# Performance work log

Measured on AMD Instinct MI355X. Metric: run time of the kernel, lower is better.

The kernel has to match this reference:

```python
import jax, jax.numpy as jnp
import numpy as np

NUM_ITERS = 5
TEMP = 0.1


def setup_inputs() -> dict:
    key = jax.random.key(0)
    k1, k2 = jax.random.split(key)
    pred_masks = jax.random.uniform(k1, (1, 100, 512, 512), dtype=jnp.float32)
    gt_masks = jax.random.uniform(k2, (50, 512, 512), dtype=jnp.float32)
    return {"pred_masks": pred_masks, "gt_masks": gt_masks}


def reference(pred_masks, gt_masks):
    # pred_masks: [B=1, K, H, W]; gt_masks: [N, H, W]
    gt = gt_masks[None]  # [1, N, H, W]
    # cost[b,k,n] = 1 - <pred_k, gt_n> over HW
    cost = 1.0 - jnp.einsum('bkhw,bnhw->bkn', pred_masks, gt)
    log_alpha = -cost / TEMP  # [1, K, N]
    for _ in range(NUM_ITERS):
        log_alpha = log_alpha - jax.nn.logsumexp(log_alpha, axis=2, keepdims=True)
        log_alpha = log_alpha - jax.nn.logsumexp(log_alpha, axis=1, keepdims=True)
    return jnp.exp(log_alpha)
```

## Files before the change

### kernel.cpp

```cpp
#include <hip/hip_runtime.h>
#include <math.h>

#define HW       262144
#define TOTSTEPS (HW / 32)
#define MROWS    100
#define NCOLS    50
#define OUTSZ    (MROWS * NCOLS)

typedef __attribute__((ext_vector_type(8))) _Float16 f16x8;
typedef __attribute__((ext_vector_type(2))) __fp16   fp16x2;
typedef __attribute__((ext_vector_type(4))) float    f32x4;

#define ABYTES   14336
#define BUFBYTES 22528

typedef __attribute__((address_space(1))) const unsigned int GU32;
typedef __attribute__((address_space(3))) unsigned int LU32;

__device__ __forceinline__ void split_f16(const float4& v0, const float4& v1,
                                          f16x8& hi, f16x8& lo) {
  float xs[8] = {v0.x, v0.y, v0.z, v0.w, v1.x, v1.y, v1.z, v1.w};
  union { fp16x2 p[4]; f16x8 v; } H, L;
#pragma unroll
  for (int j = 0; j < 4; ++j) {
    H.p[j] = __builtin_amdgcn_cvt_pkrtz(xs[2 * j], xs[2 * j + 1]);
    float l0 = xs[2 * j]     - (float)H.p[j][0];
    float l1 = xs[2 * j + 1] - (float)H.p[j][1];
    L.p[j] = __builtin_amdgcn_cvt_pkrtz(l0, l1);
  }
  hi = H.v; lo = L.v;
}

__global__ __launch_bounds__(256, 3) void dm_phase1(
    const float* __restrict__ pred, const float* __restrict__ gt,
    float* __restrict__ partial, int nblk) {
  __shared__ unsigned char smem[2 * BUFBYTES];

  const int b    = blockIdx.x;
  const int tid  = threadIdx.x;
  const int lane = tid & 63;
  const int wid  = tid >> 6;
  const int wi = wid >> 1, wj = wid & 1;
  const int g = lane >> 4, r = lane & 15;

  const int k0s = (int)(((long)b * TOTSTEPS) / nblk);
  const int k1s = (int)(((long)(b + 1) * TOTSTEPS) / nblk);
  const int nst = k1s - k0s;

  const float* srcb[6];
#pragma unroll
  for (int it = 0; it < 6; ++it) {
    int s = (it < 5) ? it * 256 + tid : 1280 + tid;
    const float* p;
    if (s < 896) {
      int row = s >> 3, t = s & 7;
      int rr = row < MROWS ? row : MROWS - 1;
      p = pred + (size_t)rr * HW + ((t ^ (row & 7)) << 2);
    } else {
      int s2 = s - 896;
      int row = s2 >> 3, t = s2 & 7;
      int rr = row < NCOLS ? row : NCOLS - 1;
      p = gt + (size_t)rr * HW + ((t ^ (row & 7)) << 2);
    }
    srcb[it] = p;
  }

  auto STAGE = [&](int q, int kf) {
    unsigned char* bufb = smem + q * BUFBYTES;
#pragma unroll
    for (int it = 0; it < 5; ++it)
      __builtin_amdgcn_global_load_lds((GU32*)(srcb[it] + kf),
          (LU32*)(bufb + (it * 256 + wid * 64) * 16), 16, 0, 0);
    if (wid < 2)
      __builtin_amdgcn_global_load_lds((GU32*)(srcb[5] + kf),
          (LU32*)(bufb + (1280 + wid * 64) * 16), 16, 0, 0);
  };

  f32x4 acc[4][2] = {};

  auto COMPUTE = [&](int q) {
    const unsigned char* bufb = smem + q * BUFBYTES;
    f16x8 bh[2], bl[2];
#pragma unroll
    for (int nf = 0; nf < 2; ++nf) {
      int R = wj * 32 + nf * 16 + r;
      const unsigned char* rowb = bufb + ABYTES + R * 128;
      float4 v0 = *(const float4*)(rowb + (((2 * g    ) ^ (r & 7)) << 4));
      float4 v1 = *(const float4*)(rowb + (((2 * g + 1) ^ (r & 7)) << 4));
      split_f16(v0, v1, bh[nf], bl[nf]);
    }
#pragma unroll
    for (int mf = 0; mf < 4; ++mf) {
      if (wi == 0 || mf < 3) {
        int R = wi * 64 + mf * 16 + r;
        const unsigned char* rowb = bufb + R * 128;
        float4 v0 = *(const float4*)(rowb + (((2 * g    ) ^ (r & 7)) << 4));
        float4 v1 = *(const float4*)(rowb + (((2 * g + 1) ^ (r & 7)) << 4));
        f16x8 ah, al;
        split_f16(v0, v1, ah, al);
#pragma unroll
        for (int nf = 0; nf < 2; ++nf) {
          acc[mf][nf] = __builtin_amdgcn_mfma_f32_16x16x32_f16(ah, bh[nf], acc[mf][nf], 0, 0, 0);
          acc[mf][nf] = __builtin_amdgcn_mfma_f32_16x16x32_f16(al, bh[nf], acc[mf][nf], 0, 0, 0);
          acc[mf][nf] = __builtin_amdgcn_mfma_f32_16x16x32_f16(ah, bl[nf], acc[mf][nf], 0, 0, 0);
        }
      }
    }
  };

  STAGE(0, k0s << 5);
  asm volatile("s_waitcnt vmcnt(0)" ::: "memory");
  __builtin_amdgcn_s_barrier();

  int q = 0;
  for (int s = 0; s < nst; ++s) {
    if (s + 1 < nst) STAGE(q ^ 1, (k0s + s + 1) << 5);
    COMPUTE(q);
    if (s + 1 < nst) asm volatile("s_waitcnt vmcnt(0)" ::: "memory");
    __builtin_amdgcn_s_barrier();
    q ^= 1;
  }

#pragma unroll
  for (int mf = 0; mf < 4; ++mf) {
#pragma unroll
    for (int nf = 0; nf < 2; ++nf) {
#pragma unroll
      for (int qq = 0; qq < 4; ++qq) {
        int row = wi * 64 + mf * 16 + g * 4 + qq;
        int col = wj * 32 + nf * 16 + r;
        if (row < MROWS && col < NCOLS)
          partial[(size_t)b * OUTSZ + row * NCOLS + col] = acc[mf][nf][qq];
      }
    }
  }
}

template <int NB>
__global__ void dm_reduce(const float* __restrict__ partial,
                          double* __restrict__ la0) {
  const int tid = threadIdx.x, wid = tid >> 6, lane = tid & 63;
  const int pbase = blockIdx.x * 16 + wid * 4;
  if (pbase >= OUTSZ) return;
  constexpr int IT = NB / 64;
  float4 v[IT];
#pragma unroll
  for (int i = 0; i < IT; ++i)
    v[i] = *(const float4*)(partial + (size_t)(lane + 64 * i) * OUTSZ + pbase);
  double d0 = 0, d1 = 0, d2 = 0, d3 = 0;
#pragma unroll
  for (int i = 0; i < IT; ++i) {
    d0 += (double)v[i].x; d1 += (double)v[i].y;
    d2 += (double)v[i].z; d3 += (double)v[i].w;
  }
#pragma unroll
  for (int off = 32; off; off >>= 1) {
    d0 += __shfl_xor(d0, off);
    d1 += __shfl_xor(d1, off);
    d2 += __shfl_xor(d2, off);
    d3 += __shfl_xor(d3, off);
  }
  if (lane == 0) {
    la0[pbase + 0] = (d0 - 1.0) * 10.0;
    la0[pbase + 1] = (d1 - 1.0) * 10.0;
    la0[pbase + 2] = (d2 - 1.0) * 10.0;
    la0[pbase + 3] = (d3 - 1.0) * 10.0;
  }
}

__global__ __launch_bounds__(256) void dm_sinkhorn(const double* __restrict__ la_in,
                                                   float* __restrict__ out) {
  __shared__ double la[OUTSZ];
  __shared__ double rp[MROWS];
  __shared__ double cp[NCOLS];
  const int t = threadIdx.x;
  for (int p = t; p < OUTSZ; p += 256) la[p] = la_in[p];
  if (t < NCOLS) cp[t] = 0.0;
  __syncthreads();
  for (int it = 0; it < 5; ++it) {
    if (t < 2 * MROWS) {
      int row = t >> 1, sl = t & 1;
      double m = -1e300;
      for (int j = sl; j < NCOLS; j += 2) m = fmax(m, la[row * NCOLS + j] - cp[j]);
      float s = 0.f;
      for (int j = sl; j < NCOLS; j += 2)
        s += __expf((float)(la[row * NCOLS + j] - cp[j] - m));
      double mo = __shfl_xor(m, 1); float so = __shfl_xor(s, 1);
      double mn = fmax(m, mo);
      s = s * __expf((float)(m - mn)) + so * __expf((float)(mo - mn));
      if (sl == 0) rp[row] = mn + (double)__logf(s);
    }
    __syncthreads();
    if (t < 4 * NCOLS) {
      int col = t >> 2, sl = t & 3;
      double m = -1e300;
      for (int i = sl; i < MROWS; i += 4) m = fmax(m, la[i * NCOLS + col] - rp[i]);
      float s = 0.f;
      for (int i = sl; i < MROWS; i += 4)
        s += __expf((float)(la[i * NCOLS + col] - rp[i] - m));
#pragma unroll
      for (int off = 1; off < 4; off <<= 1) {
        double mo = __shfl_xor(m, off); float so = __shfl_xor(s, off);
        double mn = fmax(m, mo);
        s = s * __expf((float)(m - mn)) + so * __expf((float)(mo - mn));
        m = mn;
      }
      if (sl == 0) cp[col] = m + (double)__logf(s);
    }
    __syncthreads();
  }
  for (int p = t; p < OUTSZ; p += 256)
    out[p] = __expf((float)(la[p] - rp[p / NCOLS] - cp[p % NCOLS]));
}

extern "C" void kernel_launch(void* const* d_in, const int* in_sizes, int n_in,
                              void* d_out, int out_size, void* d_ws, size_t ws_size,
                              hipStream_t stream) {
  const float* pred = (const float*)d_in[0];
  const float* gt   = (const float*)d_in[1];
  float* out = (float*)d_out;

  auto fits = [&](int nb) {
    return ((size_t)nb * OUTSZ * sizeof(float) + OUTSZ * sizeof(double)) <= ws_size;
  };
  int nblk = fits(768) ? 768 : (fits(512) ? 512 : 256);

  float*  partial = (float*)d_ws;
  double* la0 = (double*)((char*)d_ws + (size_t)nblk * OUTSZ * sizeof(float));

  dm_phase1<<<nblk, 256, 0, stream>>>(pred, gt, partial, nblk);
  if (nblk == 768)      dm_reduce<768><<<(OUTSZ + 15) / 16, 256, 0, stream>>>(partial, la0);
  else if (nblk == 512) dm_reduce<512><<<(OUTSZ + 15) / 16, 256, 0, stream>>>(partial, la0);
  else                  dm_reduce<256><<<(OUTSZ + 15) / 16, 256, 0, stream>>>(partial, la0);
  dm_sinkhorn<<<1, 256, 0, stream>>>(la0, out);
}
```

Baseline: 80.13 us.

## Triple-buffer LDS staging with prefetch depth two and trim padded rows

Replaces the double-buffered LDS pipeline with a three-stage ring. Each step now waits with vmcnt(5), so loads for step s+1 can still be in flight while step s computes. Padded rows are no longer loaded: row indices are clamped at read time, and the per-row swizzle now uses the clamped row. Staging drops from six loads per thread to five, with some filler loads landing in unused space. Grid size falls from 768 to 512 blocks and occupancy hint from 3 to 2 per CU, which fits the larger shared-memory footprint but gives less latency hiding across waves.

```diff
diff --git a/kernel.cpp b/kernel.cpp
--- a/kernel.cpp
+++ b/kernel.cpp
@@ -11,8 +11,8 @@
 typedef __attribute__((ext_vector_type(2))) __fp16   fp16x2;
 typedef __attribute__((ext_vector_type(4))) float    f32x4;
 
-#define ABYTES   14336
-#define BUFBYTES 22528
+#define ABYTES   12800
+#define BUFBYTES 20480
 
 typedef __attribute__((address_space(1))) const unsigned int GU32;
 typedef __attribute__((address_space(3))) unsigned int LU32;
@@ -31,10 +31,10 @@
   hi = H.v; lo = L.v;
 }
 
-__global__ __launch_bounds__(256, 3) void dm_phase1(
+__global__ __launch_bounds__(256, 2) void dm_phase1(
     const float* __restrict__ pred, const float* __restrict__ gt,
     float* __restrict__ partial, int nblk) {
-  __shared__ unsigned char smem[2 * BUFBYTES];
+  __shared__ unsigned char smem[3 * BUFBYTES];
 
   const int b    = blockIdx.x;
   const int tid  = threadIdx.x;
@@ -47,55 +47,52 @@
   const int k1s = (int)(((long)(b + 1) * TOTSTEPS) / nblk);
   const int nst = k1s - k0s;
 
-  const float* srcb[6];
-#pragma unroll
-  for (int it = 0; it < 6; ++it) {
-    int s = (it < 5) ? it * 256 + tid : 1280 + tid;
+  const float* srcb[5];
+#pragma unroll
+  for (int it = 0; it < 5; ++it) {
+    int s = it * 256 + tid;
     const float* p;
-    if (s < 896) {
+    if (s < 800) {
       int row = s >> 3, t = s & 7;
-      int rr = row < MROWS ? row : MROWS - 1;
-      p = pred + (size_t)rr * HW + ((t ^ (row & 7)) << 2);
+      p = pred + (size_t)row * HW + ((t ^ (row & 7)) << 2);
+    } else if (s < 1200) {
+      int s2 = s - 800;
+      int row = s2 >> 3, t = s2 & 7;
+      p = gt + (size_t)row * HW + ((t ^ (row & 7)) << 2);
     } else {
-      int s2 = s - 896;
-      int row = s2 >> 3, t = s2 & 7;
-      int rr = row < NCOLS ? row : NCOLS - 1;
-      p = gt + (size_t)rr * HW + ((t ^ (row & 7)) << 2);
+      p = pred + ((s - 1200) << 2);
     }
     srcb[it] = p;
   }
 
-  auto STAGE = [&](int q, int kf) {
-    unsigned char* bufb = smem + q * BUFBYTES;
+  auto STAGE = [&](unsigned char* bufb, int kf) {
 #pragma unroll
     for (int it = 0; it < 5; ++it)
       __builtin_amdgcn_global_load_lds((GU32*)(srcb[it] + kf),
           (LU32*)(bufb + (it * 256 + wid * 64) * 16), 16, 0, 0);
-    if (wid < 2)
-      __builtin_amdgcn_global_load_lds((GU32*)(srcb[5] + kf),
-          (LU32*)(bufb + (1280 + wid * 64) * 16), 16, 0, 0);
   };
 
   f32x4 acc[4][2] = {};
 
-  auto COMPUTE = [&](int q) {
-    const unsigned char* bufb = smem + q * BUFBYTES;
+  auto COMPUTE = [&](const unsigned char* bufb) {
     f16x8 bh[2], bl[2];
 #pragma unroll
     for (int nf = 0; nf < 2; ++nf) {
       int R = wj * 32 + nf * 16 + r;
+      if (R > NCOLS - 1) R = NCOLS - 1;
       const unsigned char* rowb = bufb + ABYTES + R * 128;
-      float4 v0 = *(const float4*)(rowb + (((2 * g    ) ^ (r & 7)) << 4));
-      float4 v1 = *(const float4*)(rowb + (((2 * g + 1) ^ (r & 7)) << 4));
+      float4 v0 = *(const float4*)(rowb + (((2 * g    ) ^ (R & 7)) << 4));
+      float4 v1 = *(const float4*)(rowb + (((2 * g + 1) ^ (R & 7)) << 4));
       split_f16(v0, v1, bh[nf], bl[nf]);
     }
 #pragma unroll
     for (int mf = 0; mf < 4; ++mf) {
       if (wi == 0 || mf < 3) {
         int R = wi * 64 + mf * 16 + r;
+        if (R > MROWS - 1) R = MROWS - 1;
         const unsigned char* rowb = bufb + R * 128;
-        float4 v0 = *(const float4*)(rowb + (((2 * g    ) ^ (r & 7)) << 4));
-        float4 v1 = *(const float4*)(rowb + (((2 * g + 1) ^ (r & 7)) << 4));
+        float4 v0 = *(const float4*)(rowb + (((2 * g    ) ^ (R & 7)) << 4));
+        float4 v1 = *(const float4*)(rowb + (((2 * g + 1) ^ (R & 7)) << 4));
         f16x8 ah, al;
         split_f16(v0, v1, ah, al);
 #pragma unroll
@@ -108,17 +105,20 @@
     }
   };
 
-  STAGE(0, k0s << 5);
-  asm volatile("s_waitcnt vmcnt(0)" ::: "memory");
-  __builtin_amdgcn_s_barrier();
-
-  int q = 0;
+  STAGE(smem, k0s << 5);
+  if (nst > 1) STAGE(smem + BUFBYTES, (k0s + 1) << 5);
+
+  int qc = 0;
   for (int s = 0; s < nst; ++s) {
-    if (s + 1 < nst) STAGE(q ^ 1, (k0s + s + 1) << 5);
-    COMPUTE(q);
-    if (s + 1 < nst) asm volatile("s_waitcnt vmcnt(0)" ::: "memory");
+    if (s + 1 < nst) asm volatile("s_waitcnt vmcnt(5)" ::: "memory");
+    else             asm volatile("s_waitcnt vmcnt(0)" ::: "memory");
     __builtin_amdgcn_s_barrier();
-    q ^= 1;
+    COMPUTE(smem + qc * BUFBYTES);
+    if (s + 2 < nst) {
+      int qs = qc + 2; if (qs >= 3) qs -= 3;
+      STAGE(smem + qs * BUFBYTES, (k0s + s + 2) << 5);
+    }
+    qc = (qc == 2) ? 0 : qc + 1;
   }
 
 #pragma unroll
@@ -223,14 +223,13 @@
   auto fits = [&](int nb) {
     return ((size_t)nb * OUTSZ * sizeof(float) + OUTSZ * sizeof(double)) <= ws_size;
   };
-  int nblk = fits(768) ? 768 : (fits(512) ? 512 : 256);
+  int nblk = fits(512) ? 512 : 256;
 
   float*  partial = (float*)d_ws;
   double* la0 = (double*)((char*)d_ws + (size_t)nblk * OUTSZ * sizeof(float));
 
   dm_phase1<<<nblk, 256, 0, stream>>>(pred, gt, partial, nblk);
-  if (nblk == 768)      dm_reduce<768><<<(OUTSZ + 15) / 16, 256, 0, stream>>>(partial, la0);
-  else if (nblk == 512) dm_reduce<512><<<(OUTSZ + 15) / 16, 256, 0, stream>>>(partial, la0);
-  else                  dm_reduce<256><<<(OUTSZ + 15) / 16, 256, 0, stream>>>(partial, la0);
+  if (nblk == 512) dm_reduce<512><<<(OUTSZ + 15) / 16, 256, 0, stream>>>(partial, la0);
+  else             dm_reduce<256><<<(OUTSZ + 15) / 16, 256, 0, stream>>>(partial, la0);
   dm_sinkhorn<<<1, 256, 0, stream>>>(la0, out);
 }
```

New measurement: 76.18 us. 4.9% less time.
